# Optimization experiments

Measured on AMD Instinct MI355X. Metric: run time of the kernel, lower is better.

## Reference

```python
import jax, jax.numpy as jnp
import numpy as np

B, S, SQ, N, DIN, H, A, O = 32, 1024, 32, 128, 128, 256, 100, 2000
MEM_COUNT, ANS_COUNT = 3, 2


def _gru_cell(x, h, w_ih, w_hh, b_ih, b_hh):
    # PyTorch GRUCell math
    gi = x @ w_ih.T + b_ih
    gh = h @ w_hh.T + b_hh
    i_r, i_z, i_n = jnp.split(gi, 3, axis=-1)
    h_r, h_z, h_n = jnp.split(gh, 3, axis=-1)
    r = jax.nn.sigmoid(i_r + h_r)
    z = jax.nn.sigmoid(i_z + h_z)
    n = jnp.tanh(i_n + r * h_n)
    return (1.0 - z) * n + z * h


def _gru_seq(x, h0, w_ih, w_hh, b_ih, b_hh):
    def step(h, xt):
        hn = _gru_cell(xt, h, w_ih, w_hh, b_ih, b_hh)
        return hn, hn
    hT, ys = jax.lax.scan(step, h0, jnp.swapaxes(x, 0, 1))
    return jnp.swapaxes(ys, 0, 1), hT


def setup_inputs() -> dict:
    key = jax.random.key(0)
    ks = iter(jax.random.split(key, 40))
    def U(shape, a=0.05):
        return jax.random.uniform(next(ks), shape, minval=-a, maxval=a, dtype=jnp.float32)
    inp = {}
    inp['c'] = jax.random.normal(next(ks), (B, S, DIN), dtype=jnp.float32)
    inp['q'] = jax.random.normal(next(ks), (B, SQ, DIN), dtype=jnp.float32)
    inp['i_state'] = jnp.zeros((1, B, H), jnp.float32)
    inp['q_state'] = jnp.zeros((1, B, H), jnp.float32)
    for p in ['in', 'qe']:
        inp[p + '_w_ih'] = U((3 * H, DIN)); inp[p + '_w_hh'] = U((3 * H, H))
        inp[p + '_b_ih'] = U((3 * H,)); inp[p + '_b_hh'] = U((3 * H,))
    inp['att_weight'] = U((H, H))
    inp['att_w1'] = U((A, 7 * H + 2)); inp['att_b1'] = U((A,))
    inp['att_w2'] = U((1, A)); inp['att_b2'] = U((1,))
    inp['mem_w_ih'] = U((3 * H, H)); inp['mem_w_hh'] = U((3 * H, H))
    inp['mem_b_ih'] = U((3 * H,)); inp['mem_b_hh'] = U((3 * H,))
    inp['out_w'] = U((O, H)); inp['out_b'] = U((O,))
    inp['ans_w_ih'] = U((3 * H, O + H)); inp['ans_w_hh'] = U((3 * H, H))
    inp['ans_b_ih'] = U((3 * H,)); inp['ans_b_hh'] = U((3 * H,))
    inp['c_index'] = jnp.sort(jax.random.randint(next(ks), (B, N), 0, S), axis=1)
    inp['len_c'] = jax.random.randint(next(ks), (B,), 1, N + 1)
    return inp


def reference(c, q, i_state, q_state, in_w_ih, in_w_hh, in_b_ih, in_b_hh,
              qe_w_ih, qe_w_hh, qe_b_ih, qe_b_hh, att_weight,
              att_w1, att_b1, att_w2, att_b2,
              mem_w_ih, mem_w_hh, mem_b_ih, mem_b_hh,
              out_w, out_b, ans_w_ih, ans_w_hh, ans_b_ih, ans_b_hh,
              c_index, len_c):
    # input / question GRU encoders (dropout omitted: eval mode)
    c_out, _ = _gru_seq(c, i_state[0], in_w_ih, in_w_hh, in_b_ih, in_b_hh)
    _, q_hT = _gru_seq(q, q_state[0], qe_w_ih, qe_w_hh, qe_b_ih, qe_b_hh)
    q_h = q_hT[:, None, :]                                   # [B,1,H]
    # gather sentence-end hidden states: [B,N,H]
    c_sel = jnp.take_along_axis(c_out, c_index[:, :, None], axis=1)
    n_sent = c_index.shape[1]
    mask = jnp.arange(n_sent)[None, :] < len_c[:, None]      # [B,N]
    cw = c_sel @ att_weight                                   # [B,N,H] (fixed across hops)
    m = q_h
    att_list = []
    for _ in range(MEM_COUNT):
        dot_q = (cw * q_h).sum(-1)                            # [B,N]
        dot_m = (cw * m).sum(-1)                              # [B,N]
        feats = jnp.concatenate([
            c_sel, jnp.broadcast_to(m, c_sel.shape), jnp.broadcast_to(q_h, c_sel.shape),
            c_sel * q_h, c_sel * m, jnp.abs(c_sel - q_h), jnp.abs(c_sel - m),
            dot_q[..., None], dot_m[..., None]], axis=2)      # [B,N,7H+2]
        h1 = jnp.tanh(feats @ att_w1.T + att_b1)
        scores = (h1 @ att_w2.T + att_b2)[..., 0]             # [B,N]
        p = jax.nn.softmax(jnp.where(mask, scores, -jnp.inf), axis=1)
        p = jnp.where(mask, p, 0.0)                           # zero-pad like pad_sequence
        att_list.append(p[..., None])
        e = (c_sel * p[..., None]).sum(1)                     # [B,H]
        m = _gru_cell(e, m[:, 0, :], mem_w_ih, mem_w_hh, mem_b_ih, mem_b_hh)[:, None, :]
    msq = m[:, 0, :]
    for _ in range(ANS_COUNT):
        y = jax.nn.softmax(msq @ out_w.T + out_b, axis=1)
        msq = _gru_cell(jnp.concatenate([y, q_hT], axis=1), msq,
                        ans_w_ih, ans_w_hh, ans_b_ih, ans_b_hh)
    y = jax.nn.softmax(msq @ out_w.T + out_b, axis=1)
    return y, jnp.stack(att_list)
```

## Files before the change

### kernel.cpp

```cpp
#include <hip/hip_runtime.h>
#include <hip/hip_bf16.h>
#include <cstdint>
#include <cstddef>

typedef short bf16x8 __attribute__((ext_vector_type(8)));
typedef float f32x4 __attribute__((ext_vector_type(4)));
typedef int   i32x4 __attribute__((ext_vector_type(4)));

#define DEV static __device__ __forceinline__

DEV unsigned short f2bf(float x){
  union{float f; unsigned int u;} v; v.f = x;
  unsigned int r = (v.u + 0x7FFFu + ((v.u>>16)&1u)) >> 16;
  return (unsigned short)r;
}
DEV float bf2f(unsigned short h){
  union{unsigned int u; float f;} v; v.u = ((unsigned int)h)<<16;
  return v.f;
}
DEV float bfsel(int dw, int hi){
  union{unsigned int u; float f;} v;
  v.u = hi ? ((unsigned int)dw & 0xFFFF0000u) : ((unsigned int)dw << 16);
  return v.f;
}
DEV float sigm_f(float x){ return __builtin_amdgcn_rcpf(1.0f + __expf(-x)); }
DEV float tanh_f(float x){ return 2.0f*__builtin_amdgcn_rcpf(1.0f + __expf(-2.0f*x)) - 1.0f; }

__global__ void k_f2bf(const float* __restrict__ src, unsigned short* __restrict__ dst, int n){
  int i = blockIdx.x*256 + threadIdx.x;
  if(i<n) dst[i] = f2bf(src[i]);
}

__global__ void k_transpose(const float* __restrict__ in, float* __restrict__ out, int R, int C){
  int i = blockIdx.x*256 + threadIdx.x;
  if(i < R*C){ int r = i/C, c = i - r*C; out[(size_t)c*R + r] = in[i]; }
}

__global__ void k_attw1(const float* __restrict__ w1, unsigned short* __restrict__ dst){
  int i = blockIdx.x*256 + threadIdx.x;
  if(i < 128*1824){
    int r = i/1824, cc = i - r*1824;
    float v = (r<100 && cc<1794)? w1[r*1794 + cc] : 0.0f;
    dst[i] = f2bf(v);
  }
}

__global__ void k_attwT(const float* __restrict__ aw, unsigned short* __restrict__ dst){
  int i = blockIdx.x*256 + threadIdx.x;
  if(i<65536){ int n = i>>8, k = i&255; dst[i] = f2bf(aw[k*256 + n]); }
}

__global__ void k_b1pad(const float* __restrict__ b1, float* __restrict__ dst){
  int i = threadIdx.x; if(i<128) dst[i] = (i<100)? b1[i] : 0.0f;
}

__global__ void k_copy(const float* __restrict__ s, float* __restrict__ d, int n){
  int i = blockIdx.x*256+threadIdx.x; if(i<n) d[i]=s[i];
}

__global__ __launch_bounds__(256) void k_gemm_bf16(
    const unsigned short* __restrict__ A, const unsigned short* __restrict__ Bt,
    int K, const float* __restrict__ bias, int act,
    float* __restrict__ outf, unsigned short* __restrict__ outbf, int ldc)
{
  int lane = threadIdx.x & 63, wave = threadIdx.x >> 6;
  int m_base = blockIdx.x*64 + (wave>>1)*32;
  int n_base = blockIdx.y*64 + (wave&1)*32;
  int cl = lane & 15, q4 = lane >> 4;
  f32x4 acc00={0.f,0.f,0.f,0.f}, acc01=acc00, acc10=acc00, acc11=acc00;
  const int kf_n = K >> 5;
  for(int kf=0; kf<kf_n; kf++){
    int ko = kf*32 + q4*8;
    bf16x8 a0 = *(const bf16x8*)(A + (size_t)(m_base+cl)*K + ko);
    bf16x8 a1 = *(const bf16x8*)(A + (size_t)(m_base+16+cl)*K + ko);
    bf16x8 b0 = *(const bf16x8*)(Bt + (size_t)(n_base+cl)*K + ko);
    bf16x8 b1 = *(const bf16x8*)(Bt + (size_t)(n_base+16+cl)*K + ko);
    acc00 = __builtin_amdgcn_mfma_f32_16x16x32_bf16(a0,b0,acc00,0,0,0);
    acc01 = __builtin_amdgcn_mfma_f32_16x16x32_bf16(a0,b1,acc01,0,0,0);
    acc10 = __builtin_amdgcn_mfma_f32_16x16x32_bf16(a1,b0,acc10,0,0,0);
    acc11 = __builtin_amdgcn_mfma_f32_16x16x32_bf16(a1,b1,acc11,0,0,0);
  }
  #pragma unroll
  for(int mt=0; mt<2; mt++){
    #pragma unroll
    for(int nt=0; nt<2; nt++){
      f32x4 av = (mt==0)? (nt==0?acc00:acc01) : (nt==0?acc10:acc11);
      int col = n_base + nt*16 + cl;
      float bv = bias? bias[col] : 0.0f;
      #pragma unroll
      for(int r=0;r<4;r++){
        int row = m_base + mt*16 + q4*4 + r;
        float v = av[r] + bv;
        if(act) v = tanh_f(v);
        if(outbf) outbf[(size_t)row*ldc + col] = f2bf(v);
        else      outf [(size_t)row*ldc + col] = v;
      }
    }
  }
}

__global__ __launch_bounds__(256) void k_gemm_gi(
    const unsigned short* __restrict__ A, const unsigned short* __restrict__ Bt,
    const float* __restrict__ bih, const float* __restrict__ bhh,
    unsigned short* __restrict__ gi_out, int ss)
{
  int lane = threadIdx.x & 63, wave = threadIdx.x >> 6;
  int m_base = blockIdx.x*64 + (wave>>1)*32;
  int n_base = blockIdx.y*64 + (wave&1)*32;
  int cl = lane & 15, q4 = lane >> 4;
  f32x4 acc00={0.f,0.f,0.f,0.f}, acc01=acc00, acc10=acc00, acc11=acc00;
  for(int kf=0; kf<4; kf++){
    int ko = kf*32 + q4*8;
    bf16x8 a0 = *(const bf16x8*)(A + (size_t)(m_base+cl)*128 + ko);
    bf16x8 a1 = *(const bf16x8*)(A + (size_t)(m_base+16+cl)*128 + ko);
    bf16x8 b0 = *(const bf16x8*)(Bt + (size_t)(n_base+cl)*128 + ko);
    bf16x8 b1 = *(const bf16x8*)(Bt + (size_t)(n_base+16+cl)*128 + ko);
    acc00 = __builtin_amdgcn_mfma_f32_16x16x32_bf16(a0,b0,acc00,0,0,0);
    acc01 = __builtin_amdgcn_mfma_f32_16x16x32_bf16(a0,b1,acc01,0,0,0);
    acc10 = __builtin_amdgcn_mfma_f32_16x16x32_bf16(a1,b0,acc10,0,0,0);
    acc11 = __builtin_amdgcn_mfma_f32_16x16x32_bf16(a1,b1,acc11,0,0,0);
  }
  const int tmask = (1<<ss) - 1;
  #pragma unroll
  for(int mt=0; mt<2; mt++){
    #pragma unroll
    for(int nt=0; nt<2; nt++){
      f32x4 av = (mt==0)? (nt==0?acc00:acc01) : (nt==0?acc10:acc11);
      int col = n_base + nt*16 + cl;
      int g = col >> 8, rem = col & 255;
      int w = rem >> 5, s = (rem>>4)&1, cl2 = rem & 15;
      float badd = bih[col] + ((g<2)? bhh[col] : 0.0f);
      #pragma unroll
      for(int r=0;r<4;r++){
        int arow = m_base + mt*16 + q4*4 + r;
        int t = arow & tmask, b = arow >> ss;
        int blk = b >> 4, brow = b & 15;
        int lane2 = (brow>>2)*16 + cl2, rc = brow & 3;
        size_t idx = ((((size_t)t*2 + blk)*8 + w)*64 + lane2)*24 + g*8 + s*4 + rc;
        gi_out[idx] = f2bf(av[r] + badd);
      }
    }
  }
}

__global__ __launch_bounds__(512,1) void k_gru_rec(
    const unsigned short* __restrict__ whh_c, const unsigned short* __restrict__ whh_q,
    const unsigned short* __restrict__ gi_c,  const unsigned short* __restrict__ gi_q,
    const float* __restrict__ bhh_c, const float* __restrict__ bhh_q,
    const float* __restrict__ h0_c,  const float* __restrict__ h0_q,
    float* __restrict__ c_hist, float* __restrict__ q_hT)
{
  __shared__ unsigned short hb0[16*264];
  __shared__ unsigned short hb1[16*264];

  const int blk = blockIdx.x;
  const bool isq = blk >= 2;
  const int cls = isq? blk-2 : blk;
  const int b0 = cls * 16;
  const unsigned short* W  = isq? whh_q : whh_c;
  const unsigned short* GI = isq? gi_q  : gi_c;
  const float* bhh = isq? bhh_q : bhh_c;
  const float* h0  = isq? h0_q  : h0_c;
  const int steps  = isq? 32 : 1024;

  const int tid = threadIdx.x;
  const int lane = tid & 63, wave = tid >> 6;
  const int cl = lane & 15, q4 = lane >> 4;

  bf16x8 Bf[3][2][8];
  #pragma unroll
  for(int g=0; g<3; g++)
    #pragma unroll
    for(int s=0; s<2; s++){
      const unsigned short* wrow = W + (size_t)(g*256 + wave*32 + s*16 + cl)*256;
      #pragma unroll
      for(int kf=0; kf<8; kf++)
        Bf[g][s][kf] = *(const bf16x8*)(wrow + kf*32 + q4*8);
    }

  float bN[2];
  #pragma unroll
  for(int s=0; s<2; s++){
    const int col = wave*32 + s*16 + cl;
    bN[s] = bhh[512+col];
  }

  f32x4 hreg[2];
  #pragma unroll
  for(int s=0; s<2; s++){
    const int col = wave*32 + s*16 + cl;
    #pragma unroll
    for(int r=0; r<4; r++){
      const int row = q4*4 + r;
      float v = h0[(size_t)(b0+row)*256 + col];
      hreg[s][r] = v;
      hb0[row*264 + col] = f2bf(v);
    }
  }
  __syncthreads();

  unsigned short* hb_rd = hb0;
  unsigned short* hb_wr = hb1;

  const unsigned short* gi_lane = GI + (((size_t)cls*8 + wave)*64 + lane)*24;
  const size_t gi_tstride = (size_t)2*8*64*24;
  float* ch_lane = c_hist + (((size_t)cls*8 + wave)*64 + lane)*8;
  const size_t ch_tstride = (size_t)2*8*64*8;

  i32x4 Gc0 = *(const i32x4*)(gi_lane);
  i32x4 Gc1 = *(const i32x4*)(gi_lane + 8);
  i32x4 Gc2 = *(const i32x4*)(gi_lane + 16);

  for(int t=0; t<steps; t++){
    const unsigned short* gpn = gi_lane + (size_t)((t+1<steps)? t+1 : t)*gi_tstride;
    i32x4 Gn0 = *(const i32x4*)(gpn);
    i32x4 Gn1 = *(const i32x4*)(gpn + 8);
    i32x4 Gn2 = *(const i32x4*)(gpn + 16);

    if(!isq && t>0){
      float* cp = ch_lane + (size_t)(t-1)*ch_tstride;
      *(f32x4*)cp       = hreg[0];
      *(f32x4*)(cp + 4) = hreg[1];
    }

    f32x4 acc[3][2];
    #pragma unroll
    for(int g=0; g<3; g++)
      #pragma unroll
      for(int s=0; s<2; s++){ f32x4 z={0.f,0.f,0.f,0.f}; acc[g][s]=z; }
    #pragma unroll
    for(int kf=0; kf<8; kf++){
      bf16x8 a = *(const bf16x8*)&hb_rd[cl*264 + kf*32 + q4*8];
      #pragma unroll
      for(int g=0; g<3; g++)
        #pragma unroll
        for(int s=0; s<2; s++)
          acc[g][s] = __builtin_amdgcn_mfma_f32_16x16x32_bf16(a, Bf[g][s][kf], acc[g][s], 0,0,0);
    }

    #pragma unroll
    for(int s=0; s<2; s++){
      const int col = wave*32 + s*16 + cl;
      float x4[4];
      #pragma unroll
      for(int r=0; r<4; r++){
        const int k = s*4 + r;
        float rr = sigm_f(bfsel(Gc0[k>>1], k&1) + acc[0][s][r]);
        float zz = sigm_f(bfsel(Gc1[k>>1], k&1) + acc[1][s][r]);
        float nn = tanh_f(bfsel(Gc2[k>>1], k&1) + rr*(acc[2][s][r] + bN[s]));
        float x  = nn + zz*(hreg[s][r] - nn);
        hreg[s][r] = x;
        x4[r] = x;
      }
      #pragma unroll
      for(int p=0; p<2; p++){
        __hip_bfloat162 bb = __float22bfloat162_rn(make_float2(x4[2*p], x4[2*p+1]));
        union{ __hip_bfloat162 b; unsigned int u; } cvt; cvt.b = bb;
        const int row = q4*4 + 2*p;
        hb_wr[row*264 + col]     = (unsigned short)(cvt.u & 0xFFFFu);
        hb_wr[(row+1)*264 + col] = (unsigned short)(cvt.u >> 16);
      }
    }
    __syncthreads();
    unsigned short* tmp = hb_rd; hb_rd = hb_wr; hb_wr = tmp;
    Gc0 = Gn0; Gc1 = Gn1; Gc2 = Gn2;
  }

  if(!isq){
    float* cp = ch_lane + (size_t)(steps-1)*ch_tstride;
    *(f32x4*)cp       = hreg[0];
    *(f32x4*)(cp + 4) = hreg[1];
  } else {
    #pragma unroll
    for(int s=0; s<2; s++){
      const int col = wave*32 + s*16 + cl;
      #pragma unroll
      for(int r=0; r<4; r++)
        q_hT[(size_t)(b0+q4*4+r)*256 + col] = hreg[s][r];
    }
  }
}

__global__ void k_gather(const float* __restrict__ c_hist, const int* __restrict__ c_index,
                         float* __restrict__ c_sel, unsigned short* __restrict__ c_sel_bf){
  int row = blockIdx.x;
  int b = row >> 7, s = row & 127;
  int idx = c_index[b*128 + s];
  int col = threadIdx.x;
  int cls = b >> 4, brow = b & 15;
  int q4 = brow >> 2, rI = brow & 3;
  int w = col >> 5, sI = (col>>4)&1, cl = col & 15;
  size_t addr = (size_t)idx*8192 + (size_t)cls*4096 + w*512 + (q4*16+cl)*8 + sI*4 + rI;
  float v = c_hist[addr];
  c_sel   [(size_t)row*256 + col] = v;
  c_sel_bf[(size_t)row*256 + col] = f2bf(v);
}

__global__ void k_feats(const float* __restrict__ c_sel, const float* __restrict__ cw,
                        const float* __restrict__ m_, const float* __restrict__ qh,
                        unsigned short* __restrict__ feats){
  int row = blockIdx.x, tid = threadIdx.x;
  int b = row >> 7;
  float cs  = c_sel[(size_t)row*256 + tid];
  float mj  = m_[b*256 + tid];
  float qj  = qh[b*256 + tid];
  float cwj = cw[(size_t)row*256 + tid];
  float dq = cwj*qj, dm = cwj*mj;
  #pragma unroll
  for(int o=32;o>0;o>>=1){ dq += __shfl_down(dq,o); dm += __shfl_down(dm,o); }
  __shared__ float rq[4], rm[4];
  int lane = tid&63, wave=tid>>6;
  if(lane==0){ rq[wave]=dq; rm[wave]=dm; }
  __syncthreads();
  unsigned short* fr = feats + (size_t)row*1824;
  fr[tid]      = f2bf(cs);
  fr[256+tid]  = f2bf(mj);
  fr[512+tid]  = f2bf(qj);
  fr[768+tid]  = f2bf(cs*qj);
  fr[1024+tid] = f2bf(cs*mj);
  fr[1280+tid] = f2bf(fabsf(cs-qj));
  fr[1536+tid] = f2bf(fabsf(cs-mj));
  if(tid==0){
    float DQ = rq[0]+rq[1]+rq[2]+rq[3];
    float DM = rm[0]+rm[1]+rm[2]+rm[3];
    fr[1792]=f2bf(DQ); fr[1793]=f2bf(DM);
  }
  if(tid<30) fr[1794+tid]=0;
}

__global__ void k_scores(const float* __restrict__ h1, const float* __restrict__ w2,
                         const float* __restrict__ b2, float* __restrict__ scores){
  int row = blockIdx.x*4 + (threadIdx.x>>6);
  int lane = threadIdx.x & 63;
  float v = 0.0f;
  if(lane < 100)    v += h1[(size_t)row*128 + lane]*w2[lane];
  if(lane+64 < 100) v += h1[(size_t)row*128 + lane+64]*w2[lane+64];
  #pragma unroll
  for(int o=32;o>0;o>>=1) v += __shfl_down(v,o);
  if(lane==0) scores[row] = v + b2[0];
}

__global__ void k_softmax_e(const float* __restrict__ scores, const int* __restrict__ len_c,
                            const float* __restrict__ c_sel, float* __restrict__ out_att,
                            float* __restrict__ e){
  __shared__ float red[256];
  __shared__ float p[128];
  int b = blockIdx.x, tid = threadIdx.x;
  int L = len_c[b];
  float s = -1e30f;
  if(tid<128 && tid<L) s = scores[b*128+tid];
  red[tid]=s; __syncthreads();
  for(int o=128;o>0;o>>=1){ if(tid<o) red[tid]=fmaxf(red[tid],red[tid+o]); __syncthreads(); }
  float mx = red[0]; __syncthreads();
  float ex = (tid<128 && tid<L)? __expf(s-mx) : 0.0f;
  red[tid]=ex; __syncthreads();
  for(int o=128;o>0;o>>=1){ if(tid<o) red[tid]+=red[tid+o]; __syncthreads(); }
  float inv = 1.0f/red[0];
  if(tid<128){ float pv = ex*inv; p[tid]=pv; out_att[b*128+tid]=pv; }
  __syncthreads();
  float acc = 0.0f;
  for(int si=0; si<128; si++) acc += p[si]*c_sel[((size_t)b*128+si)*256 + tid];
  e[b*256+tid] = acc;
}

__global__ void k_gru_cell(const float* __restrict__ x1, int len1,
                           const float* __restrict__ x2, int len2,
                           const float* __restrict__ hprev,
                           const float* __restrict__ wihT, const float* __restrict__ whhT,
                           const float* __restrict__ bih, const float* __restrict__ bhh,
                           float* __restrict__ hout){
  __shared__ float xs[2304];
  __shared__ float hs[256];
  int m = blockIdx.x, tid = threadIdx.x;
  int Kx = len1 + len2;
  for(int i=tid;i<len1;i+=256) xs[i] = x1[(size_t)m*len1 + i];
  for(int i=tid;i<len2;i+=256) xs[len1+i] = x2[(size_t)m*len2 + i];
  hs[tid] = hprev[m*256 + tid];
  __syncthreads();
  float ar=0, az=0, an=0;
  for(int k=0;k<Kx;k++){
    float xv = xs[k];
    const float* wr = wihT + (size_t)k*768;
    ar += xv*wr[tid]; az += xv*wr[256+tid]; an += xv*wr[512+tid];
  }
  float gr=0, gz=0, gn=0;
  for(int k=0;k<256;k++){
    float hv = hs[k];
    const float* wr = whhT + (size_t)k*768;
    gr += hv*wr[tid]; gz += hv*wr[256+tid]; gn += hv*wr[512+tid];
  }
  float rr = sigm_f(ar + bih[tid]     + gr + bhh[tid]);
  float zz = sigm_f(az + bih[256+tid] + gz + bhh[256+tid]);
  float nn = tanh_f(an + bih[512+tid] + rr*(gn + bhh[512+tid]));
  hout[m*256+tid] = (1.0f-zz)*nn + zz*hs[tid];
}

__global__ void k_logits(const float* __restrict__ msq, const float* __restrict__ out_wT,
                         const float* __restrict__ out_b, float* __restrict__ ylin){
  int i = blockIdx.x*256 + threadIdx.x;
  if(i >= 32*2000) return;
  int mrow = i/2000, n = i - mrow*2000;
  float acc = out_b[n];
  const float* mr = msq + mrow*256;
  for(int k=0;k<256;k++) acc += mr[k]*out_wT[(size_t)k*2000 + n];
  ylin[i] = acc;
}

__global__ void k_softmax_o(const float* __restrict__ x, float* __restrict__ y){
  __shared__ float red[256];
  int b = blockIdx.x, tid = threadIdx.x;
  const float* xr = x + (size_t)b*2000;
  float mx = -1e30f;
  for(int i=tid;i<2000;i+=256) mx = fmaxf(mx, xr[i]);
  red[tid]=mx; __syncthreads();
  for(int o=128;o>0;o>>=1){ if(tid<o) red[tid]=fmaxf(red[tid],red[tid+o]); __syncthreads(); }
  mx = red[0]; __syncthreads();
  float sum=0.0f;
  for(int i=tid;i<2000;i+=256) sum += __expf(xr[i]-mx);
  red[tid]=sum; __syncthreads();
  for(int o=128;o>0;o>>=1){ if(tid<o) red[tid]+=red[tid+o]; __syncthreads(); }
  float inv = 1.0f/red[0];
  for(int i=tid;i<2000;i+=256) y[(size_t)b*2000+i] = __expf(xr[i]-mx)*inv;
}

extern "C" void kernel_launch(void* const* d_in, const int* in_sizes, int n_in,
                              void* d_out, int out_size, void* d_ws, size_t ws_size,
                              hipStream_t stream)
{
  const float* c        = (const float*)d_in[0];
  const float* q        = (const float*)d_in[1];
  const float* i_state  = (const float*)d_in[2];
  const float* q_state  = (const float*)d_in[3];
  const float* in_w_ih  = (const float*)d_in[4];
  const float* in_w_hh  = (const float*)d_in[5];
  const float* in_b_ih  = (const float*)d_in[6];
  const float* in_b_hh  = (const float*)d_in[7];
  const float* qe_w_ih  = (const float*)d_in[8];
  const float* qe_w_hh  = (const float*)d_in[9];
  const float* qe_b_ih  = (const float*)d_in[10];
  const float* qe_b_hh  = (const float*)d_in[11];
  const float* att_weight = (const float*)d_in[12];
  const float* att_w1   = (const float*)d_in[13];
  const float* att_b1   = (const float*)d_in[14];
  const float* att_w2   = (const float*)d_in[15];
  const float* att_b2   = (const float*)d_in[16];
  const float* mem_w_ih = (const float*)d_in[17];
  const float* mem_w_hh = (const float*)d_in[18];
  const float* mem_b_ih = (const float*)d_in[19];
  const float* mem_b_hh = (const float*)d_in[20];
  const float* out_w    = (const float*)d_in[21];
  const float* out_b    = (const float*)d_in[22];
  const float* ans_w_ih = (const float*)d_in[23];
  const float* ans_w_hh = (const float*)d_in[24];
  const float* ans_b_ih = (const float*)d_in[25];
  const float* ans_b_hh = (const float*)d_in[26];
  const int*   c_index  = (const int*)d_in[27];
  const int*   len_c    = (const int*)d_in[28];
  float* outp = (float*)d_out;

  char* wp = (char*)d_ws;
  auto take = [&](size_t nbytes)->char*{
    char* p = wp; wp += (nbytes + 255) & ~(size_t)255; return p;
  };
  unsigned short* c_bf      = (unsigned short*)take((size_t)32*1024*128*2);
  unsigned short* q_bf      = (unsigned short*)take((size_t)32*32*128*2);
  unsigned short* wih_in_bf = (unsigned short*)take(768*128*2);
  unsigned short* wih_qe_bf = (unsigned short*)take(768*128*2);
  unsigned short* whh_in_bf = (unsigned short*)take(768*256*2);
  unsigned short* whh_qe_bf = (unsigned short*)take(768*256*2);
  unsigned short* attwT_bf  = (unsigned short*)take(256*256*2);
  unsigned short* attw1_bf  = (unsigned short*)take(128*1824*2);
  float* b1pad              = (float*)take(128*4);
  float* out_wT             = (float*)take((size_t)256*2000*4);
  float* mem_wihT           = (float*)take(256*768*4);
  float* mem_whhT           = (float*)take(256*768*4);
  float* ans_wihT           = (float*)take((size_t)2256*768*4);
  float* ans_whhT           = (float*)take(256*768*4);
  unsigned short* gi_c_bf   = (unsigned short*)take((size_t)32768*768*2);
  unsigned short* gi_q_bf   = (unsigned short*)take((size_t)1024*768*2);
  float* c_hist             = (float*)take((size_t)1024*8192*4);
  float* q_hT               = (float*)take(32*256*4);
  float* c_sel              = (float*)take((size_t)4096*256*4);
  unsigned short* c_sel_bf  = (unsigned short*)take((size_t)4096*256*2);
  float* cw                 = (float*)take((size_t)4096*256*4);
  unsigned short* feats_bf  = (unsigned short*)take((size_t)4096*1824*2);
  float* h1                 = (float*)take((size_t)4096*128*4);
  float* scores             = (float*)take(4096*4);
  float* e_buf              = (float*)take(32*256*4);
  float* m_buf              = (float*)take(32*256*4);
  float* msq                = (float*)take(32*256*4);
  float* ylin               = (float*)take((size_t)32*2000*4);
  float* ybuf               = (float*)take((size_t)32*2000*4);

  k_f2bf<<<16384,256,0,stream>>>(c, c_bf, 32*1024*128);
  k_f2bf<<<512,256,0,stream>>>(q, q_bf, 32*32*128);
  k_f2bf<<<384,256,0,stream>>>(in_w_ih, wih_in_bf, 768*128);
  k_f2bf<<<384,256,0,stream>>>(qe_w_ih, wih_qe_bf, 768*128);
  k_f2bf<<<768,256,0,stream>>>(in_w_hh, whh_in_bf, 768*256);
  k_f2bf<<<768,256,0,stream>>>(qe_w_hh, whh_qe_bf, 768*256);
  k_attwT<<<256,256,0,stream>>>(att_weight, attwT_bf);
  k_attw1<<<912,256,0,stream>>>(att_w1, attw1_bf);
  k_b1pad<<<1,128,0,stream>>>(att_b1, b1pad);
  k_transpose<<<2000,256,0,stream>>>(out_w, out_wT, 2000, 256);
  k_transpose<<<768,256,0,stream>>>(mem_w_ih, mem_wihT, 768, 256);
  k_transpose<<<768,256,0,stream>>>(mem_w_hh, mem_whhT, 768, 256);
  k_transpose<<<6768,256,0,stream>>>(ans_w_ih, ans_wihT, 768, 2256);
  k_transpose<<<768,256,0,stream>>>(ans_w_hh, ans_whhT, 768, 256);

  k_gemm_gi<<<dim3(512,12),256,0,stream>>>(c_bf, wih_in_bf, in_b_ih, in_b_hh, gi_c_bf, 10);
  k_gemm_gi<<<dim3(16,12),256,0,stream>>>(q_bf, wih_qe_bf, qe_b_ih, qe_b_hh, gi_q_bf, 5);

  k_gru_rec<<<4,512,0,stream>>>(whh_in_bf, whh_qe_bf, gi_c_bf, gi_q_bf,
                                in_b_hh, qe_b_hh, i_state, q_state, c_hist, q_hT);

  k_gather<<<4096,256,0,stream>>>(c_hist, c_index, c_sel, c_sel_bf);
  k_gemm_bf16<<<dim3(64,4),256,0,stream>>>(c_sel_bf, attwT_bf, 256, nullptr, 0, cw, nullptr, 256);
  k_copy<<<32,256,0,stream>>>(q_hT, m_buf, 32*256);

  for(int it=0; it<3; it++){
    k_feats<<<4096,256,0,stream>>>(c_sel, cw, m_buf, q_hT, feats_bf);
    k_gemm_bf16<<<dim3(64,2),256,0,stream>>>(feats_bf, attw1_bf, 1824, b1pad, 1, h1, nullptr, 128);
    k_scores<<<1024,256,0,stream>>>(h1, att_w2, att_b2, scores);
    k_softmax_e<<<32,256,0,stream>>>(scores, len_c, c_sel, outp + 64000 + it*4096, e_buf);
    k_gru_cell<<<32,256,0,stream>>>(e_buf, 256, nullptr, 0, m_buf,
                                    mem_wihT, mem_whhT, mem_b_ih, mem_b_hh, m_buf);
  }

  k_copy<<<32,256,0,stream>>>(m_buf, msq, 32*256);
  for(int it=0; it<2; it++){
    k_logits<<<250,256,0,stream>>>(msq, out_wT, out_b, ylin);
    k_softmax_o<<<32,256,0,stream>>>(ylin, ybuf);
    k_gru_cell<<<32,256,0,stream>>>(ybuf, 2000, q_hT, 256, msq,
                                    ans_wihT, ans_whhT, ans_b_ih, ans_b_hh, msq);
  }
  k_logits<<<250,256,0,stream>>>(msq, out_wT, out_b, ylin);
  k_softmax_o<<<32,256,0,stream>>>(ylin, outp);
}
```

Before: 3.117 ms.

## Split GRU recurrence over 16 waves with one column tile each

The recurrent GRU kernel now runs 1024 threads (16 waves) per block instead of 512, so each wave owns one 16-column tile rather than two. Each wave issues half as many MFMAs per step and holds half the weight fragments in registers. The gi and c_hist layouts, plus the gather indexing, change to match the new per-wave tiling, and the n-gate hidden bias is folded into the accumulator's initial value. The next-step gi prefetch is dropped in favour of loading gi inside each step, which puts global-load latency back on the serial path. Each step's barrier now also has to synchronise twice as many waves.

```diff
diff --git a/kernel.cpp b/kernel.cpp
--- a/kernel.cpp
+++ b/kernel.cpp
@@ -6,6 +6,7 @@
 typedef short bf16x8 __attribute__((ext_vector_type(8)));
 typedef float f32x4 __attribute__((ext_vector_type(4)));
 typedef int   i32x4 __attribute__((ext_vector_type(4)));
+typedef int   i32x2 __attribute__((ext_vector_type(2)));
 
 #define DEV static __device__ __forceinline__
 
@@ -128,22 +129,22 @@
       f32x4 av = (mt==0)? (nt==0?acc00:acc01) : (nt==0?acc10:acc11);
       int col = n_base + nt*16 + cl;
       int g = col >> 8, rem = col & 255;
-      int w = rem >> 5, s = (rem>>4)&1, cl2 = rem & 15;
+      int w = rem >> 4, cl2 = rem & 15;
       float badd = bih[col] + ((g<2)? bhh[col] : 0.0f);
       #pragma unroll
       for(int r=0;r<4;r++){
         int arow = m_base + mt*16 + q4*4 + r;
         int t = arow & tmask, b = arow >> ss;
-        int blk = b >> 4, brow = b & 15;
+        int cls = b >> 4, brow = b & 15;
         int lane2 = (brow>>2)*16 + cl2, rc = brow & 3;
-        size_t idx = ((((size_t)t*2 + blk)*8 + w)*64 + lane2)*24 + g*8 + s*4 + rc;
+        size_t idx = ((((size_t)t*2 + cls)*16 + w)*64 + lane2)*12 + g*4 + rc;
         gi_out[idx] = f2bf(av[r] + badd);
       }
     }
   }
 }
 
-__global__ __launch_bounds__(512,1) void k_gru_rec(
+__global__ __launch_bounds__(1024,1) void k_gru_rec(
     const unsigned short* __restrict__ whh_c, const unsigned short* __restrict__ whh_q,
     const unsigned short* __restrict__ gi_c,  const unsigned short* __restrict__ gi_q,
     const float* __restrict__ bhh_c, const float* __restrict__ bhh_q,
@@ -166,118 +167,83 @@
   const int tid = threadIdx.x;
   const int lane = tid & 63, wave = tid >> 6;
   const int cl = lane & 15, q4 = lane >> 4;
-
-  bf16x8 Bf[3][2][8];
+  const int col = wave*16 + cl;
+
+  bf16x8 Bf[3][8];
   #pragma unroll
-  for(int g=0; g<3; g++)
-    #pragma unroll
-    for(int s=0; s<2; s++){
-      const unsigned short* wrow = W + (size_t)(g*256 + wave*32 + s*16 + cl)*256;
-      #pragma unroll
-      for(int kf=0; kf<8; kf++)
-        Bf[g][s][kf] = *(const bf16x8*)(wrow + kf*32 + q4*8);
-    }
-
-  float bN[2];
+  for(int g=0; g<3; g++){
+    const unsigned short* wrow = W + (size_t)(g*256 + col)*256;
+    #pragma unroll
+    for(int kf=0; kf<8; kf++)
+      Bf[g][kf] = *(const bf16x8*)(wrow + kf*32 + q4*8);
+  }
+
+  const float bN = bhh[512+col];
+
+  f32x4 hreg;
   #pragma unroll
-  for(int s=0; s<2; s++){
-    const int col = wave*32 + s*16 + cl;
-    bN[s] = bhh[512+col];
-  }
-
-  f32x4 hreg[2];
-  #pragma unroll
-  for(int s=0; s<2; s++){
-    const int col = wave*32 + s*16 + cl;
-    #pragma unroll
-    for(int r=0; r<4; r++){
-      const int row = q4*4 + r;
-      float v = h0[(size_t)(b0+row)*256 + col];
-      hreg[s][r] = v;
-      hb0[row*264 + col] = f2bf(v);
-    }
+  for(int r=0; r<4; r++){
+    const int row = q4*4 + r;
+    float v = h0[(size_t)(b0+row)*256 + col];
+    hreg[r] = v;
+    hb0[row*264 + col] = f2bf(v);
   }
   __syncthreads();
 
   unsigned short* hb_rd = hb0;
   unsigned short* hb_wr = hb1;
 
-  const unsigned short* gi_lane = GI + (((size_t)cls*8 + wave)*64 + lane)*24;
-  const size_t gi_tstride = (size_t)2*8*64*24;
-  float* ch_lane = c_hist + (((size_t)cls*8 + wave)*64 + lane)*8;
-  const size_t ch_tstride = (size_t)2*8*64*8;
-
-  i32x4 Gc0 = *(const i32x4*)(gi_lane);
-  i32x4 Gc1 = *(const i32x4*)(gi_lane + 8);
-  i32x4 Gc2 = *(const i32x4*)(gi_lane + 16);
+  const unsigned short* gi_lane = GI + (((size_t)cls*16 + wave)*64 + lane)*12;
+  const unsigned gi_tstride = 2*16*64*12;
+  float* ch_lane = c_hist + (size_t)cls*4096 + (wave*64 + lane)*4;
 
   for(int t=0; t<steps; t++){
-    const unsigned short* gpn = gi_lane + (size_t)((t+1<steps)? t+1 : t)*gi_tstride;
-    i32x4 Gn0 = *(const i32x4*)(gpn);
-    i32x4 Gn1 = *(const i32x4*)(gpn + 8);
-    i32x4 Gn2 = *(const i32x4*)(gpn + 16);
-
-    if(!isq && t>0){
-      float* cp = ch_lane + (size_t)(t-1)*ch_tstride;
-      *(f32x4*)cp       = hreg[0];
-      *(f32x4*)(cp + 4) = hreg[1];
-    }
-
-    f32x4 acc[3][2];
-    #pragma unroll
-    for(int g=0; g<3; g++)
-      #pragma unroll
-      for(int s=0; s<2; s++){ f32x4 z={0.f,0.f,0.f,0.f}; acc[g][s]=z; }
+    const unsigned short* gp = gi_lane + (size_t)t*gi_tstride;
+    i32x2 G0 = *(const i32x2*)(gp);
+    i32x2 G1 = *(const i32x2*)(gp + 4);
+    i32x2 G2 = *(const i32x2*)(gp + 8);
+
+    if(!isq && t>0)
+      *(f32x4*)(ch_lane + (size_t)(t-1)*8192) = hreg;
+
+    f32x4 acc0={0.f,0.f,0.f,0.f}, acc1=acc0;
+    f32x4 acc2={bN,bN,bN,bN};
     #pragma unroll
     for(int kf=0; kf<8; kf++){
       bf16x8 a = *(const bf16x8*)&hb_rd[cl*264 + kf*32 + q4*8];
-      #pragma unroll
-      for(int g=0; g<3; g++)
-        #pragma unroll
-        for(int s=0; s<2; s++)
-          acc[g][s] = __builtin_amdgcn_mfma_f32_16x16x32_bf16(a, Bf[g][s][kf], acc[g][s], 0,0,0);
+      acc0 = __builtin_amdgcn_mfma_f32_16x16x32_bf16(a, Bf[0][kf], acc0, 0,0,0);
+      acc1 = __builtin_amdgcn_mfma_f32_16x16x32_bf16(a, Bf[1][kf], acc1, 0,0,0);
+      acc2 = __builtin_amdgcn_mfma_f32_16x16x32_bf16(a, Bf[2][kf], acc2, 0,0,0);
     }
 
-    #pragma unroll
-    for(int s=0; s<2; s++){
-      const int col = wave*32 + s*16 + cl;
-      float x4[4];
-      #pragma unroll
-      for(int r=0; r<4; r++){
-        const int k = s*4 + r;
-        float rr = sigm_f(bfsel(Gc0[k>>1], k&1) + acc[0][s][r]);
-        float zz = sigm_f(bfsel(Gc1[k>>1], k&1) + acc[1][s][r]);
-        float nn = tanh_f(bfsel(Gc2[k>>1], k&1) + rr*(acc[2][s][r] + bN[s]));
-        float x  = nn + zz*(hreg[s][r] - nn);
-        hreg[s][r] = x;
-        x4[r] = x;
-      }
-      #pragma unroll
-      for(int p=0; p<2; p++){
-        __hip_bfloat162 bb = __float22bfloat162_rn(make_float2(x4[2*p], x4[2*p+1]));
-        union{ __hip_bfloat162 b; unsigned int u; } cvt; cvt.b = bb;
-        const int row = q4*4 + 2*p;
-        hb_wr[row*264 + col]     = (unsigned short)(cvt.u & 0xFFFFu);
-        hb_wr[(row+1)*264 + col] = (unsigned short)(cvt.u >> 16);
-      }
+    float x4[4];
+    #pragma unroll
+    for(int r=0; r<4; r++){
+      float rr = sigm_f(bfsel(G0[r>>1], r&1) + acc0[r]);
+      float zz = sigm_f(bfsel(G1[r>>1], r&1) + acc1[r]);
+      float nn = tanh_f(bfsel(G2[r>>1], r&1) + rr*acc2[r]);
+      float x  = nn + zz*(hreg[r] - nn);
+      hreg[r] = x;
+      x4[r] = x;
+    }
+    #pragma unroll
+    for(int p=0; p<2; p++){
+      __hip_bfloat162 bb = __float22bfloat162_rn(make_float2(x4[2*p], x4[2*p+1]));
+      union{ __hip_bfloat162 b; unsigned int u; } cvt; cvt.b = bb;
+      const int row = q4*4 + 2*p;
+      hb_wr[row*264 + col]     = (unsigned short)(cvt.u & 0xFFFFu);
+      hb_wr[(row+1)*264 + col] = (unsigned short)(cvt.u >> 16);
     }
     __syncthreads();
     unsigned short* tmp = hb_rd; hb_rd = hb_wr; hb_wr = tmp;
-    Gc0 = Gn0; Gc1 = Gn1; Gc2 = Gn2;
   }
 
   if(!isq){
-    float* cp = ch_lane + (size_t)(steps-1)*ch_tstride;
-    *(f32x4*)cp       = hreg[0];
-    *(f32x4*)(cp + 4) = hreg[1];
+    *(f32x4*)(ch_lane + (size_t)(steps-1)*8192) = hreg;
   } else {
     #pragma unroll
-    for(int s=0; s<2; s++){
-      const int col = wave*32 + s*16 + cl;
-      #pragma unroll
-      for(int r=0; r<4; r++)
-        q_hT[(size_t)(b0+q4*4+r)*256 + col] = hreg[s][r];
-    }
+    for(int r=0; r<4; r++)
+      q_hT[(size_t)(b0+q4*4+r)*256 + col] = hreg[r];
   }
 }
 
@@ -289,8 +255,8 @@
   int col = threadIdx.x;
   int cls = b >> 4, brow = b & 15;
   int q4 = brow >> 2, rI = brow & 3;
-  int w = col >> 5, sI = (col>>4)&1, cl = col & 15;
-  size_t addr = (size_t)idx*8192 + (size_t)cls*4096 + w*512 + (q4*16+cl)*8 + sI*4 + rI;
+  int w = col >> 4, cl = col & 15;
+  size_t addr = (size_t)idx*8192 + (size_t)cls*4096 + (w*64 + q4*16 + cl)*4 + rI;
   float v = c_hist[addr];
   c_sel   [(size_t)row*256 + col] = v;
   c_sel_bf[(size_t)row*256 + col] = f2bf(v);
@@ -510,8 +476,8 @@
   k_gemm_gi<<<dim3(512,12),256,0,stream>>>(c_bf, wih_in_bf, in_b_ih, in_b_hh, gi_c_bf, 10);
   k_gemm_gi<<<dim3(16,12),256,0,stream>>>(q_bf, wih_qe_bf, qe_b_ih, qe_b_hh, gi_q_bf, 5);
 
-  k_gru_rec<<<4,512,0,stream>>>(whh_in_bf, whh_qe_bf, gi_c_bf, gi_q_bf,
-                                in_b_hh, qe_b_hh, i_state, q_state, c_hist, q_hT);
+  k_gru_rec<<<4,1024,0,stream>>>(whh_in_bf, whh_qe_bf, gi_c_bf, gi_q_bf,
+                                 in_b_hh, qe_b_hh, i_state, q_state, c_hist, q_hT);
 
   k_gather<<<4096,256,0,stream>>>(c_hist, c_index, c_sel, c_sel_bf);
   k_gemm_bf16<<<dim3(64,4),256,0,stream>>>(c_sel_bf, attwT_bf, 256, nullptr, 0, cw, nullptr, 256);
```

Measured after the change: 3.401 ms. 1.09x slower.

## Fold exp2 scaling constants into GRU weights and biases, drop gi prefetch

Applied to the files above, without the earlier changes.

Pre-scales the recurrent W_hh weights, the gi projections and the n-gate bias by -log2(e) or -2·log2(e), so the gate nonlinearities in the serial recurrence become a raw exp2 plus a reciprocal with no per-element multiply. The n-gate bias is folded into the accumulator initialisation. The MFMA loop is split into two passes over the s halves, and the gi register prefetch for the next step is replaced by a load at the start of each step. This shortens the latency-bound per-step critical path but exposes the gi load latency and adds a little bf16 rounding of the scaled values.

```diff
diff --git a/kernel.cpp b/kernel.cpp
--- a/kernel.cpp
+++ b/kernel.cpp
@@ -9,6 +9,9 @@
 
 #define DEV static __device__ __forceinline__
 
+#define SRZ (-1.4426950408889634f)
+#define SN  (-2.8853900817779268f)
+
 DEV unsigned short f2bf(float x){
   union{float f; unsigned int u;} v; v.f = x;
   unsigned int r = (v.u + 0x7FFFu + ((v.u>>16)&1u)) >> 16;
@@ -23,12 +26,27 @@
   v.u = hi ? ((unsigned int)dw & 0xFFFF0000u) : ((unsigned int)dw << 16);
   return v.f;
 }
+DEV float fexp2(float x){
+#if __has_builtin(__builtin_amdgcn_exp2f)
+  return __builtin_amdgcn_exp2f(x);
+#else
+  float r; asm("v_exp_f32 %0, %1" : "=v"(r) : "v"(x)); return r;
+#endif
+}
 DEV float sigm_f(float x){ return __builtin_amdgcn_rcpf(1.0f + __expf(-x)); }
 DEV float tanh_f(float x){ return 2.0f*__builtin_amdgcn_rcpf(1.0f + __expf(-2.0f*x)) - 1.0f; }
 
 __global__ void k_f2bf(const float* __restrict__ src, unsigned short* __restrict__ dst, int n){
   int i = blockIdx.x*256 + threadIdx.x;
   if(i<n) dst[i] = f2bf(src[i]);
+}
+
+__global__ void k_whh(const float* __restrict__ src, unsigned short* __restrict__ dst){
+  int i = blockIdx.x*256 + threadIdx.x;
+  if(i < 768*256){
+    float s = (i < 512*256)? SRZ : SN;
+    dst[i] = f2bf(src[i]*s);
+  }
 }
 
 __global__ void k_transpose(const float* __restrict__ in, float* __restrict__ out, int R, int C){
@@ -130,14 +148,15 @@
       int g = col >> 8, rem = col & 255;
       int w = rem >> 5, s = (rem>>4)&1, cl2 = rem & 15;
       float badd = bih[col] + ((g<2)? bhh[col] : 0.0f);
+      float scale = (g<2)? SRZ : SN;
       #pragma unroll
       for(int r=0;r<4;r++){
         int arow = m_base + mt*16 + q4*4 + r;
         int t = arow & tmask, b = arow >> ss;
-        int blk = b >> 4, brow = b & 15;
+        int cls = b >> 4, brow = b & 15;
         int lane2 = (brow>>2)*16 + cl2, rc = brow & 3;
-        size_t idx = ((((size_t)t*2 + blk)*8 + w)*64 + lane2)*24 + g*8 + s*4 + rc;
-        gi_out[idx] = f2bf(av[r] + badd);
+        size_t idx = ((((size_t)t*2 + cls)*8 + w)*64 + lane2)*24 + g*8 + s*4 + rc;
+        gi_out[idx] = f2bf((av[r] + badd)*scale);
       }
     }
   }
@@ -182,7 +201,7 @@
   #pragma unroll
   for(int s=0; s<2; s++){
     const int col = wave*32 + s*16 + cl;
-    bN[s] = bhh[512+col];
+    bN[s] = bhh[512+col]*SN;
   }
 
   f32x4 hreg[2];
@@ -207,15 +226,11 @@
   float* ch_lane = c_hist + (((size_t)cls*8 + wave)*64 + lane)*8;
   const size_t ch_tstride = (size_t)2*8*64*8;
 
-  i32x4 Gc0 = *(const i32x4*)(gi_lane);
-  i32x4 Gc1 = *(const i32x4*)(gi_lane + 8);
-  i32x4 Gc2 = *(const i32x4*)(gi_lane + 16);
-
   for(int t=0; t<steps; t++){
-    const unsigned short* gpn = gi_lane + (size_t)((t+1<steps)? t+1 : t)*gi_tstride;
-    i32x4 Gn0 = *(const i32x4*)(gpn);
-    i32x4 Gn1 = *(const i32x4*)(gpn + 8);
-    i32x4 Gn2 = *(const i32x4*)(gpn + 16);
+    const unsigned short* gp = gi_lane + (size_t)t*gi_tstride;
+    i32x4 G0 = *(const i32x4*)(gp);
+    i32x4 G1 = *(const i32x4*)(gp + 8);
+    i32x4 G2 = *(const i32x4*)(gp + 16);
 
     if(!isq && t>0){
       float* cp = ch_lane + (size_t)(t-1)*ch_tstride;
@@ -227,15 +242,25 @@
     #pragma unroll
     for(int g=0; g<3; g++)
       #pragma unroll
-      for(int s=0; s<2; s++){ f32x4 z={0.f,0.f,0.f,0.f}; acc[g][s]=z; }
+      for(int s=0; s<2; s++){
+        f32x4 z={0.f,0.f,0.f,0.f};
+        if(g==2){ z[0]=bN[s]; z[1]=bN[s]; z[2]=bN[s]; z[3]=bN[s]; }
+        acc[g][s]=z;
+      }
+
     #pragma unroll
     for(int kf=0; kf<8; kf++){
       bf16x8 a = *(const bf16x8*)&hb_rd[cl*264 + kf*32 + q4*8];
-      #pragma unroll
-      for(int g=0; g<3; g++)
-        #pragma unroll
-        for(int s=0; s<2; s++)
-          acc[g][s] = __builtin_amdgcn_mfma_f32_16x16x32_bf16(a, Bf[g][s][kf], acc[g][s], 0,0,0);
+      acc[0][0] = __builtin_amdgcn_mfma_f32_16x16x32_bf16(a, Bf[0][0][kf], acc[0][0], 0,0,0);
+      acc[1][0] = __builtin_amdgcn_mfma_f32_16x16x32_bf16(a, Bf[1][0][kf], acc[1][0], 0,0,0);
+      acc[2][0] = __builtin_amdgcn_mfma_f32_16x16x32_bf16(a, Bf[2][0][kf], acc[2][0], 0,0,0);
+    }
+    #pragma unroll
+    for(int kf=0; kf<8; kf++){
+      bf16x8 a = *(const bf16x8*)&hb_rd[cl*264 + kf*32 + q4*8];
+      acc[0][1] = __builtin_amdgcn_mfma_f32_16x16x32_bf16(a, Bf[0][1][kf], acc[0][1], 0,0,0);
+      acc[1][1] = __builtin_amdgcn_mfma_f32_16x16x32_bf16(a, Bf[1][1][kf], acc[1][1], 0,0,0);
+      acc[2][1] = __builtin_amdgcn_mfma_f32_16x16x32_bf16(a, Bf[2][1][kf], acc[2][1], 0,0,0);
     }
 
     #pragma unroll
@@ -245,9 +270,9 @@
       #pragma unroll
       for(int r=0; r<4; r++){
         const int k = s*4 + r;
-        float rr = sigm_f(bfsel(Gc0[k>>1], k&1) + acc[0][s][r]);
-        float zz = sigm_f(bfsel(Gc1[k>>1], k&1) + acc[1][s][r]);
-        float nn = tanh_f(bfsel(Gc2[k>>1], k&1) + rr*(acc[2][s][r] + bN[s]));
+        float rr = __builtin_amdgcn_rcpf(1.0f + fexp2(bfsel(G0[k>>1],k&1) + acc[0][s][r]));
+        float zz = __builtin_amdgcn_rcpf(1.0f + fexp2(bfsel(G1[k>>1],k&1) + acc[1][s][r]));
+        float nn = 2.0f*__builtin_amdgcn_rcpf(1.0f + fexp2(bfsel(G2[k>>1],k&1) + rr*acc[2][s][r])) - 1.0f;
         float x  = nn + zz*(hreg[s][r] - nn);
         hreg[s][r] = x;
         x4[r] = x;
@@ -263,7 +288,6 @@
     }
     __syncthreads();
     unsigned short* tmp = hb_rd; hb_rd = hb_wr; hb_wr = tmp;
-    Gc0 = Gn0; Gc1 = Gn1; Gc2 = Gn2;
   }
 
   if(!isq){
@@ -496,8 +520,8 @@
   k_f2bf<<<512,256,0,stream>>>(q, q_bf, 32*32*128);
   k_f2bf<<<384,256,0,stream>>>(in_w_ih, wih_in_bf, 768*128);
   k_f2bf<<<384,256,0,stream>>>(qe_w_ih, wih_qe_bf, 768*128);
-  k_f2bf<<<768,256,0,stream>>>(in_w_hh, whh_in_bf, 768*256);
-  k_f2bf<<<768,256,0,stream>>>(qe_w_hh, whh_qe_bf, 768*256);
+  k_whh<<<768,256,0,stream>>>(in_w_hh, whh_in_bf);
+  k_whh<<<768,256,0,stream>>>(qe_w_hh, whh_qe_bf);
   k_attwT<<<256,256,0,stream>>>(att_weight, attwT_bf);
   k_attw1<<<912,256,0,stream>>>(att_w1, attw1_bf);
   k_b1pad<<<1,128,0,stream>>>(att_b1, b1pad);
```

Result: slower. 3.837 ms (+23.1%).
